# Kernel optimization log

Measured on AMD Instinct MI355X. Metric: run time of the kernel, lower is better.

## Reference

```python
import jax, jax.numpy as jnp
import numpy as np

K = 24            # neighbors
RBF_KERNELS = 16
RBF_GAMMA = 10.0
CUTOFF = 5.0
BN_EPS = 1e-5


def setup_inputs() -> dict:
    key = jax.random.key(0)
    ks = jax.random.split(key, 6)
    B, C, N = 16, 32, 2048
    x = jax.random.normal(ks[0], (B, C, N), dtype=jnp.float32)
    idx_base = (jnp.arange(B, dtype=jnp.int64) * N).reshape(B, 1, 1)
    att_w1 = jax.random.normal(ks[1], (64, 2 * C + RBF_KERNELS), dtype=jnp.float32) * 0.1
    att_w2 = jax.random.normal(ks[2], (1, 64), dtype=jnp.float32) * 0.1
    upd_w = jax.random.normal(ks[3], (64, C), dtype=jnp.float32) * 0.1
    bn_gamma = jnp.ones((64,), dtype=jnp.float32)
    bn_beta = jnp.zeros((64,), dtype=jnp.float32)
    res_w = jax.random.normal(ks[4], (64, C), dtype=jnp.float32) * 0.1
    return {"x": x, "idx_base": idx_base, "att_w1": att_w1, "att_w2": att_w2,
            "upd_w": upd_w, "bn_gamma": bn_gamma, "bn_beta": bn_beta, "res_w": res_w}


def _forward(x, att_w1, att_w2, upd_w, bn_gamma, bn_beta, res_w):
    B, C, N = x.shape
    centers = jnp.linspace(0.0, CUTOFF, RBF_KERNELS).astype(x.dtype)
    # pair[b,i,j] = -||x_i - x_j||^2  (negative squared distance)
    xx = jnp.sum(x * x, axis=1)                          # [B,N]
    dots = jnp.einsum('bcn,bcm->bnm', x, x)              # [B,N,N]
    pair = 2.0 * dots - xx[:, :, None] - xx[:, None, :]
    neg_d2, idx = jax.lax.top_k(pair, K)                 # [B,N,K] nearest neighbors
    dist = jnp.sqrt(jnp.maximum(-neg_d2, 1e-12))         # [B,N,K]
    xt = jnp.transpose(x, (0, 2, 1))                     # [B,N,C]
    neigh = xt[jnp.arange(B)[:, None, None], idx]        # [B,N,K,C] gather
    cent = jnp.broadcast_to(xt[:, :, None, :], (B, N, K, C))
    # RBF expansion of neighbor distances
    diff = dist[..., None] - centers                     # [B,N,K,RBF]
    rbf = jnp.clip(jnp.exp(-RBF_GAMMA * diff * diff), 1e-10, 1.0)
    # attention MLP (1x1 convs == per-edge dense layers)
    att_in = jnp.concatenate([cent, neigh, rbf], axis=-1)          # [B,N,K,2C+RBF]
    h = jax.nn.leaky_relu(jnp.einsum('bnkf,of->bnko', att_in, att_w1), 0.2)
    logits = jnp.einsum('bnko,o->bnk', h, att_w2[0])               # [B,N,K]
    att = jax.nn.softmax(logits, axis=-1)                          # softmax over K neighbors
    weighted = att[..., None] * neigh                              # [B,N,K,C]
    # update_ff: conv1x1 -> BatchNorm2d (batch stats over B,N,K) -> LeakyReLU(0.02)
    upd = jnp.einsum('bnkc,oc->bnko', weighted, upd_w)             # [B,N,K,64]
    mean = jnp.mean(upd, axis=(0, 1, 2))
    var = jnp.mean((upd - mean) ** 2, axis=(0, 1, 2))
    upd = (upd - mean) * jax.lax.rsqrt(var + BN_EPS) * bn_gamma + bn_beta
    upd = jax.nn.leaky_relu(upd, 0.02)
    res = jnp.einsum('bnkc,oc->bnko', neigh, res_w)                # residual projection
    feat = jnp.mean(upd + 0.1 * res, axis=2)                       # mean over K -> [B,N,64]
    return jnp.transpose(feat, (0, 2, 1))                          # [B,64,N]


def reference(x, idx_base, att_w1, att_w2, upd_w, bn_gamma, bn_beta, res_w):
    # idx_base is only needed for torch's flattened-gather trick; the per-batch
    # advanced-index gather above computes identical math.
    return _forward(x, att_w1, att_w2, upd_w, bn_gamma, bn_beta, res_w)
```

## Files before the change

kernel.cpp:

```cpp
#include <hip/hip_runtime.h>
#include <math.h>

#define B_   16
#define C_   32
#define N_   2048
#define K_   24
#define BNK_ (B_*N_*K_)

typedef float vf2 __attribute__((ext_vector_type(2)));
typedef __attribute__((ext_vector_type(8))) short bf16x8;
typedef __attribute__((ext_vector_type(4))) float f32x4;

#define WS_XT   0u
#define WS_XXD  1048576u
#define WS_XXF  1114112u
#define WS_IDX  1146880u
#define WS_D2   1933312u
#define WS_ATT  2719744u
#define WS_LOG  3506176u
#define WS_ST   4292608u
#define WS_AB   4292736u
#define WS_W    4292864u
#define WS_W2   4325632u
#define WS_Y    4358400u
#define WS_L    4358400u
#define WS_HL   10649856u

__device__ __forceinline__ unsigned short bf16rne(float f) {
  unsigned int u = __float_as_uint(f);
  return (unsigned short)((u + 0x7FFFu + ((u >> 16) & 1u)) >> 16);
}

__global__ __launch_bounds__(256) void k0_prep(const float* __restrict__ x,
                                               float* __restrict__ ws) {
  const int i = blockIdx.x;
  const int xcd = i & 7, j = i >> 3;
  const int b = 2 * xcd + (j & 1);
  const int half = j >> 1;
  const int t = (b << 11) + (half << 8) + threadIdx.x;
  const int n = t & 2047;
  const float* xp = x + ((size_t)b * C_ * N_) + n;
  float4* xt4 = (float4*)(ws + WS_XT + (size_t)t * C_);
  uint4*  hl  = (uint4*)(ws + WS_HL) + (size_t)t * 8;
  unsigned int hu[16], lu[16];
  double s = 0.0;
#pragma unroll
  for (int cg = 0; cg < 8; ++cg) {
    float4 v;
    v.x = xp[(size_t)(4*cg  ) * N_];
    v.y = xp[(size_t)(4*cg+1) * N_];
    v.z = xp[(size_t)(4*cg+2) * N_];
    v.w = xp[(size_t)(4*cg+3) * N_];
    xt4[cg] = v;
    s = fma((double)v.x, (double)v.x, s);
    s = fma((double)v.y, (double)v.y, s);
    s = fma((double)v.z, (double)v.z, s);
    s = fma((double)v.w, (double)v.w, s);
    unsigned short h0 = bf16rne(v.x), h1 = bf16rne(v.y);
    unsigned short h2 = bf16rne(v.z), h3 = bf16rne(v.w);
    float l0 = v.x - __uint_as_float((unsigned int)h0 << 16);
    float l1 = v.y - __uint_as_float((unsigned int)h1 << 16);
    float l2 = v.z - __uint_as_float((unsigned int)h2 << 16);
    float l3 = v.w - __uint_as_float((unsigned int)h3 << 16);
    hu[2*cg]   = (unsigned int)h0 | ((unsigned int)h1 << 16);
    hu[2*cg+1] = (unsigned int)h2 | ((unsigned int)h3 << 16);
    lu[2*cg]   = (unsigned int)bf16rne(l0) | ((unsigned int)bf16rne(l1) << 16);
    lu[2*cg+1] = (unsigned int)bf16rne(l2) | ((unsigned int)bf16rne(l3) << 16);
  }
#pragma unroll
  for (int q = 0; q < 4; ++q) {
    uint4 hv; hv.x = hu[4*q]; hv.y = hu[4*q+1]; hv.z = hu[4*q+2]; hv.w = hu[4*q+3];
    hl[q] = hv;
    uint4 lv; lv.x = lu[4*q]; lv.y = lu[4*q+1]; lv.z = lu[4*q+2]; lv.w = lu[4*q+3];
    hl[4+q] = lv;
  }
  ((double*)(ws + WS_XXD))[t] = s;
  ws[WS_XXF + t] = -0.5f * (float)s;
  ws[WS_W + t] = 0.f;
  ws[WS_W2 + t] = 0.f;
  if (t < 128) ws[WS_ST + t] = 0.f;
}

__global__ __launch_bounds__(256, 8) void k1a_mfma(float* __restrict__ ws) {
  __shared__ unsigned short tl[2][1024];
  const int lane = threadIdx.x & 63;
  const int wv   = __builtin_amdgcn_readfirstlane(threadIdx.x >> 6);
  const int i = blockIdx.x;
  const int xcd = i & 7, j = i >> 3;
  const int b = 2 * xcd + (j & 1);
  const int j2 = j >> 1;
  const int nblk = j2 >> 2;
  const int mq   = j2 & 3;
  const int l16 = lane & 15, lg = lane >> 4;

  const unsigned short* HL = (const unsigned short*)(ws + WS_HL) + ((size_t)b << 17);
  const int nrow = (nblk << 6) + (wv << 4) + l16;
  const bf16x8 bh = *(const bf16x8*)(HL + ((size_t)nrow << 6) + (lg << 3));
  const bf16x8 bl = *(const bf16x8*)(HL + ((size_t)nrow << 6) + 32 + (lg << 3));

  const int mbase = mq << 9;
  const float4* nxx = (const float4*)(ws + WS_XXF + (b << 11) + mbase);

  const int srow = lane >> 3;
  const int sslot = (lane & 7) ^ srow;
  const unsigned short* Sp = HL + ((size_t)(mbase + srow) << 6) + (sslot << 3);

  const int ah_off = (l16 << 6) + (((lg    ) ^ (l16 & 7)) << 3);
  const int al_off = (l16 << 6) + (((4 | lg) ^ (l16 & 7)) << 3);

  if (wv == 0) {
    __builtin_amdgcn_global_load_lds(
        (const __attribute__((address_space(1))) unsigned int*)(const void*)Sp,
        (__attribute__((address_space(3))) unsigned int*)(void*)&tl[0][0], 16, 0, 0);
    __builtin_amdgcn_global_load_lds(
        (const __attribute__((address_space(1))) unsigned int*)(const void*)(Sp + 512),
        (__attribute__((address_space(3))) unsigned int*)(void*)&tl[0][512], 16, 0, 0);
  }
  __syncthreads();

  float val[12];
#pragma unroll
  for (int j0 = 0; j0 < 12; ++j0) val[j0] = -3.4e38f;
  int id = mbase + (lg << 2);

#pragma unroll 2
  for (int t = 0; t < 32; ++t) {
    const int cur = t & 1;
    if (t < 31 && wv == (t & 3)) {
      const unsigned short* sp = Sp + ((size_t)(t + 1) << 10);
      __builtin_amdgcn_global_load_lds(
          (const __attribute__((address_space(1))) unsigned int*)(const void*)sp,
          (__attribute__((address_space(3))) unsigned int*)(void*)&tl[cur ^ 1][0], 16, 0, 0);
      __builtin_amdgcn_global_load_lds(
          (const __attribute__((address_space(1))) unsigned int*)(const void*)(sp + 512),
          (__attribute__((address_space(3))) unsigned int*)(void*)&tl[cur ^ 1][512], 16, 0, 0);
    }
    bf16x8 ah = *(const bf16x8*)(&tl[cur][ah_off]);
    bf16x8 al = *(const bf16x8*)(&tl[cur][al_off]);
    float4 xq = nxx[(t << 2) + lg];
    f32x4 acc;
    acc[0] = xq.x; acc[1] = xq.y; acc[2] = xq.z; acc[3] = xq.w;
    acc = __builtin_amdgcn_mfma_f32_16x16x32_bf16(ah, bh, acc, 0, 0, 0);
    acc = __builtin_amdgcn_mfma_f32_16x16x32_bf16(al, bh, acc, 0, 0, 0);
    acc = __builtin_amdgcn_mfma_f32_16x16x32_bf16(ah, bl, acc, 0, 0, 0);
#pragma unroll
    for (int r = 0; r < 4; ++r) {
      int sb = (__float_as_int(acc[r]) & ~2047) | (id + r);
      float sp2 = __int_as_float(sb);
#pragma unroll
      for (int j0 = 11; j0 >= 1; --j0)
        val[j0] = __builtin_amdgcn_fmed3f(val[j0 - 1], val[j0], sp2);
      val[0] = fmaxf(val[0], sp2);
    }
    id += 16;
    __syncthreads();
  }
  const int pg = (b << 5) + nblk;
  float* Lp = ws + WS_L +
      (((size_t)pg * 16 + (mq << 2) + lg) * 12) * 64 + (wv << 4) + l16;
#pragma unroll
  for (int j0 = 0; j0 < 12; ++j0) Lp[(size_t)j0 * 64] = val[j0];
}

__global__ __launch_bounds__(64) void k1b_sel(float* __restrict__ ws) {
  const float* xt = ws + WS_XT;
  const double* xxd = (const double*)(ws + WS_XXD);
  const int lane = threadIdx.x & 63;
  const int i = blockIdx.x;
  const int xcd = i & 7, j = i >> 3;
  const int b = 2 * xcd + (j & 1);
  const int sub = j >> 1;
  const int pg = (b << 5) + sub;
  const int bn = (b << 11) + (sub << 6) + lane;

  float val[28];
#pragma unroll
  for (int j0 = 0; j0 < 28; ++j0) val[j0] = -3.4e38f;
  const float* Lp = ws + WS_L + ((size_t)pg * 16 * 12) * 64 + lane;
#pragma unroll 4
  for (int t = 0; t < 192; ++t) {
    float sp = Lp[(size_t)t * 64];
#pragma unroll
    for (int j0 = 27; j0 >= 1; --j0)
      val[j0] = __builtin_amdgcn_fmed3f(val[j0 - 1], val[j0], sp);
    val[0] = fmaxf(val[0], sp);
  }

  double xnd[C_];
  {
    const float* p = xt + (size_t)bn * C_;
#pragma unroll
    for (int c = 0; c < C_; ++c) xnd[c] = (double)p[c];
  }
  double dl[K_];
#pragma unroll
  for (int j0 = 0; j0 < K_; ++j0) dl[j0] = -1.7e308;

#pragma unroll 1
  for (int j0 = 0; j0 < 28; ++j0) {
    const int m = __float_as_int(val[j0]) & 2047;
    const float* r = xt + ((size_t)((b << 11) + m)) * C_;
    double a0 = 0.0, a1 = 0.0;
#pragma unroll
    for (int c = 0; c < 16; ++c) {
      a0 = fma((double)r[c],      xnd[c],      a0);
      a1 = fma((double)r[c + 16], xnd[c + 16], a1);
    }
    double s = 2.0 * (a0 + a1) - xxd[(b << 11) + m];
    long long bits = (__double_as_longlong(s) & 0xFFFFFFFFFFFFF800ll) | (long long)m;
    double sp = __longlong_as_double(bits);
    if (sp > dl[K_ - 1]) {
      bool c2 = true;
#pragma unroll
      for (int jj = K_ - 1; jj >= 1; --jj) {
        bool c1 = sp > dl[jj - 1];
        dl[jj] = c1 ? dl[jj - 1] : (c2 ? sp : dl[jj]);
        c2 = c1;
      }
      if (c2) dl[0] = sp;
    }
  }

  int*   op = (int*)ws + WS_IDX + (size_t)bn * K_;
  float* dp = ws + WS_D2 + (size_t)bn * K_;
  const double xxn = xxd[bn];
#pragma unroll
  for (int rr = 0; rr < K_; ++rr) {
    long long bl = __double_as_longlong(dl[rr]);
    op[rr] = (int)(bl & 0x7FFll);
    dp[rr] = (float)(xxn - __longlong_as_double(bl & 0xFFFFFFFFFFFFF800ll));
  }
}

__global__ __launch_bounds__(256) void kY(const float* __restrict__ w1,
                                          const float* __restrict__ updw,
                                          const float* __restrict__ resw,
                                          float* __restrict__ ws) {
  const int lane = threadIdx.x & 63;
  const int wv   = __builtin_amdgcn_readfirstlane(threadIdx.x >> 6);
  const int i = blockIdx.x;
  const int xcd = i & 7, j = i >> 3;
  const int b = 2 * xcd + (j & 1);
  const int j2 = j >> 1;
  const int slot = (j2 << 2) | wv;
  const int s  = slot & 7;
  const int pg = slot >> 3;
  const int p = (b << 11) + (pg << 6) + lane;
  const float* xt = ws + WS_XT;

  float row[C_];
  {
    const float4* rp = (const float4*)(xt + (size_t)p * C_);
#pragma unroll
    for (int q = 0; q < 8; ++q) {
      float4 v = rp[q];
      row[4*q] = v.x; row[4*q+1] = v.y; row[4*q+2] = v.z; row[4*q+3] = v.w;
    }
  }
  const int part = s >> 1;
  const int hch  = (s & 1) * 32;
  const float* W   = (part == 0) ? w1 : (part == 1) ? (w1 + 32)
                   : (part == 2) ? updw : resw;
  const int stride = (part < 2) ? 80 : 32;
  float* yp = ws + WS_Y + (size_t)p * 256 + s * 32;
#pragma unroll 2
  for (int og = 0; og < 8; ++og) {
    float a[4] = {0.f, 0.f, 0.f, 0.f};
#pragma unroll
    for (int u = 0; u < 4; ++u) {
      const float* wr = W + (hch + 4 * og + u) * stride;
#pragma unroll
      for (int c = 0; c < C_; ++c) a[u] = fmaf(row[c], wr[c], a[u]);
    }
    float4 st; st.x = a[0]; st.y = a[1]; st.z = a[2]; st.w = a[3];
    ((float4*)yp)[og] = st;
  }
}

__global__ __launch_bounds__(256, 4) void k2_logits(const float* __restrict__ w1,
                                                    const float* __restrict__ w2,
                                                    float* __restrict__ ws) {
  const int lane = threadIdx.x & 63;
  const int wv   = __builtin_amdgcn_readfirstlane(threadIdx.x >> 6);
  const int s = lane & 15, g = lane >> 4;
  const int i = blockIdx.x;
  const int xcd = i & 7, j = i >> 3;
  const int b = 2 * xcd + (j & 1);
  const int grp = j >> 1;
  const int bn = (b << 11) + (grp << 4) + (wv << 2) + g;
  const float* Y = ws + WS_Y;

  float w1r[4][16], w2r[4], ba[4];
#pragma unroll
  for (int e = 0; e < 4; ++e) {
    const int o = 4 * s + e;
    w2r[e] = w2[o];
#pragma unroll
    for (int q = 0; q < 4; ++q) {
      float4 v = *(const float4*)(w1 + o * 80 + 64 + 4 * q);
      w1r[e][4*q] = v.x; w1r[e][4*q+1] = v.y; w1r[e][4*q+2] = v.z; w1r[e][4*q+3] = v.w;
    }
  }
  {
    float4 v = *(const float4*)(Y + (size_t)bn * 256 + 4 * s);
    ba[0] = v.x; ba[1] = v.y; ba[2] = v.z; ba[3] = v.w;
  }

  const int*   ip = (const int*)ws + WS_IDX + (size_t)bn * K_;
  const float* dp = ws + WS_D2 + (size_t)bn * K_;

#pragma unroll 2
  for (int k = 0; k < K_; ++k) {
    const int mk  = ip[k];
    const float dd = dp[k];
    const float dist = sqrtf(fmaxf(dd, 1e-12f));
    float4 rv = *(const float4*)(Y + (size_t)((b << 11) + mk) * 256 + 64 + 4 * s);
    float a0 = ba[0] + rv.x, a1 = ba[1] + rv.y, a2 = ba[2] + rv.z, a3 = ba[3] + rv.w;
#pragma unroll
    for (int r = 0; r < 16; ++r) {
      float t = dist - (float)r * (5.0f / 15.0f);
      float e = __expf(-10.f * t * t);
      float rb = fminf(fmaxf(e, 1e-10f), 1.0f);
      a0 = fmaf(rb, w1r[0][r], a0);
      a1 = fmaf(rb, w1r[1][r], a1);
      a2 = fmaf(rb, w1r[2][r], a2);
      a3 = fmaf(rb, w1r[3][r], a3);
    }
    a0 = fmaxf(a0, 0.2f * a0); a1 = fmaxf(a1, 0.2f * a1);
    a2 = fmaxf(a2, 0.2f * a2); a3 = fmaxf(a3, 0.2f * a3);
    float p = a0 * w2r[0];
    p = fmaf(a1, w2r[1], p);
    p = fmaf(a2, w2r[2], p);
    p = fmaf(a3, w2r[3], p);
    p += __shfl_xor(p, 1);
    p += __shfl_xor(p, 2);
    p += __shfl_xor(p, 4);
    p += __shfl_xor(p, 8);
    if (s == 0) ws[WS_LOG + (size_t)k * 32768 + bn] = p;
  }
}

__global__ __launch_bounds__(256) void k2_softmax(float* __restrict__ ws) {
  __shared__ float h[4096];
  const int i = blockIdx.x;
  const int xcd = i & 7, j = i >> 3;
  const int b = 2 * xcd + (j & 1);
  const int half = j >> 1;
  const int bn = (b << 11) + (half << 8) + threadIdx.x;

#pragma unroll
  for (int q = 0; q < 16; ++q) h[threadIdx.x + (q << 8)] = 0.f;
  __syncthreads();

  float l[K_];
#pragma unroll
  for (int k = 0; k < K_; ++k) l[k] = ws[WS_LOG + (size_t)k * 32768 + bn];
  float mx = l[0];
#pragma unroll
  for (int k = 1; k < K_; ++k) mx = fmaxf(mx, l[k]);
  float den = 0.f;
#pragma unroll
  for (int k = 0; k < K_; ++k) { l[k] = __expf(l[k] - mx); den += l[k]; }
  const float inv = 1.f / den;
#pragma unroll
  for (int k = 0; k < K_; ++k) l[k] *= inv;

  float4* ap = (float4*)(ws + WS_ATT + (size_t)bn * K_);
#pragma unroll
  for (int q = 0; q < 6; ++q) {
    float4 v; v.x = l[4*q]; v.y = l[4*q+1]; v.z = l[4*q+2]; v.w = l[4*q+3];
    ap[q] = v;
  }
  const int* ip = (const int*)ws + WS_IDX + (size_t)bn * K_;
#pragma unroll
  for (int k = 0; k < K_; ++k) {
    const int mk = ip[k];
    atomicAdd(&h[mk], l[k]);
    atomicAdd(&h[2048 + mk], l[k] * l[k]);
  }
  __syncthreads();
#pragma unroll
  for (int q = 0; q < 8; ++q) {
    const int m = threadIdx.x + (q << 8);
    atomicAdd(ws + WS_W  + (b << 11) + m, h[m]);
    atomicAdd(ws + WS_W2 + (b << 11) + m, h[2048 + m]);
  }
}

__global__ __launch_bounds__(256) void k2b_stats(float* __restrict__ ws) {
  __shared__ float ls[128];
  const int lane = threadIdx.x & 63;
  const int wv   = __builtin_amdgcn_readfirstlane(threadIdx.x >> 6);
  if (threadIdx.x < 128) ls[threadIdx.x] = 0.f;
  __syncthreads();
  const int i = blockIdx.x;
  const int xcd = i & 7, j = i >> 3;
  const int b = 2 * xcd + (j & 1);
  const int half = j >> 1;
  const float* Y = ws + WS_Y;
  float s1 = 0.f, s2 = 0.f;
#pragma unroll 1
  for (int it = 0; it < 64; ++it) {
    const int m = (b << 11) + (half << 8) + (wv << 6) + it;
    const float w  = ws[WS_W + m];
    const float w2 = ws[WS_W2 + m];
    const float yv = Y[(size_t)m * 256 + 128 + lane];
    s1 = fmaf(w, yv, s1);
    s2 = fmaf(w2, yv * yv, s2);
  }
  atomicAdd(&ls[lane], s1);
  atomicAdd(&ls[64 + lane], s2);
  __syncthreads();
  if (threadIdx.x < 128) atomicAdd(ws + WS_ST + threadIdx.x, ls[threadIdx.x]);
}

__global__ __launch_bounds__(256) void k4_out(float* __restrict__ out,
                                              const float* __restrict__ gam,
                                              const float* __restrict__ bet,
                                              const float* __restrict__ ws) {
  __shared__ float tile[32][65];
  const int lane = threadIdx.x & 63;
  const int wv   = __builtin_amdgcn_readfirstlane(threadIdx.x >> 6);
  const int i = blockIdx.x;
  const int xcd = i & 7, j = i >> 3;
  const int b = 2 * xcd + (j & 1);
  const int j2 = j >> 1;
  const int n0 = j2 << 5;
  const float* Y = ws + WS_Y;

  float A, Bb;
  {
    const float s1 = ws[WS_ST + lane], s2 = ws[WS_ST + 64 + lane];
    const float cnt = (float)BNK_;
    const float mean = s1 / cnt;
    const float var = fmaxf(s2 / cnt - mean * mean, 0.f);
    A = gam[lane] / sqrtf(var + 1e-5f);
    Bb = bet[lane] - mean * A;
  }

#pragma unroll 1
  for (int pt = 0; pt < 8; ++pt) {
    const int bn = (b << 11) + n0 + (wv << 3) + pt;
    const int*   ip = (const int*)ws + WS_IDX + (size_t)bn * K_;
    const float* ap = ws + WS_ATT + (size_t)bn * K_;
    float facc = 0.f, racc = 0.f;
#pragma unroll
    for (int k = 0; k < K_; ++k) {
      const int mk = ip[k];
      const float* row = Y + (size_t)((b << 11) + mk) * 256;
      float yv = row[128 + lane];
      float rv = row[192 + lane];
      float u = ap[k] * yv;
      float v = fmaf(u, A, Bb);
      v = v > 0.f ? v : 0.02f * v;
      facc += v;
      racc += rv;
    }
    tile[(wv << 3) + pt][lane] = (facc + 0.1f * racc) * (1.f / 24.f);
  }
  __syncthreads();
  const int o = threadIdx.x >> 2, q = threadIdx.x & 3;
  float* op = out + ((size_t)(b * 64 + o)) * 2048 + n0 + q * 8;
  float4 v0, v1;
  v0.x = tile[q*8+0][o]; v0.y = tile[q*8+1][o]; v0.z = tile[q*8+2][o]; v0.w = tile[q*8+3][o];
  v1.x = tile[q*8+4][o]; v1.y = tile[q*8+5][o]; v1.z = tile[q*8+6][o]; v1.w = tile[q*8+7][o];
  ((float4*)op)[0] = v0;
  ((float4*)op)[1] = v1;
}

extern "C" void kernel_launch(void* const* d_in, const int* in_sizes, int n_in,
                              void* d_out, int out_size, void* d_ws, size_t ws_size,
                              hipStream_t stream) {
  (void)in_sizes; (void)n_in; (void)out_size; (void)ws_size;
  const float* x    = (const float*)d_in[0];
  const float* w1   = (const float*)d_in[2];
  const float* w2   = (const float*)d_in[3];
  const float* updw = (const float*)d_in[4];
  const float* bng  = (const float*)d_in[5];
  const float* bnb  = (const float*)d_in[6];
  const float* resw = (const float*)d_in[7];
  float* out = (float*)d_out;
  float* ws  = (float*)d_ws;

  k0_prep  <<<dim3(128),  dim3(256), 0, stream>>>(x, ws);
  k1a_mfma <<<dim3(2048), dim3(256), 0, stream>>>(ws);
  k1b_sel  <<<dim3(512),  dim3(64),  0, stream>>>(ws);
  kY       <<<dim3(1024), dim3(256), 0, stream>>>(w1, updw, resw, ws);
  k2_logits<<<dim3(2048), dim3(256), 0, stream>>>(w1, w2, ws);
  k2_softmax<<<dim3(128), dim3(256), 0, stream>>>(ws);
  k2b_stats<<<dim3(128),  dim3(256), 0, stream>>>(ws);
  k4_out   <<<dim3(1024), dim3(256), 0, stream>>>(out, bng, bnb, ws);
}
```

Baseline: 348.2 us.

## Deduplicate RBF expansion in logits kernel via per-wave shared memory

k2_logits is remapped so each lane owns one of the 64 hidden channels and a wave handles its 4 points one after another. Each point's 24×16 RBF values are computed once per wave, stored in LDS and read back as float4 broadcasts. Before, the 16 lanes serving a point each recomputed every exp, so this removes that redundant transcendental work and cuts register use. It costs a longer serial loop per wave, a full 64-lane shuffle reduction per neighbor, and reliance on in-wave LDS ordering with no barrier; occupancy is also raised to 8 blocks per CU.

```diff
diff --git a/kernel.cpp b/kernel.cpp
--- a/kernel.cpp
+++ b/kernel.cpp
@@ -277,66 +277,68 @@
   }
 }
 
-__global__ __launch_bounds__(256, 4) void k2_logits(const float* __restrict__ w1,
+__global__ __launch_bounds__(256, 8) void k2_logits(const float* __restrict__ w1,
                                                     const float* __restrict__ w2,
                                                     float* __restrict__ ws) {
+  __shared__ float dist_s[4][24];
+  __shared__ float rbf_s[4][384];
   const int lane = threadIdx.x & 63;
   const int wv   = __builtin_amdgcn_readfirstlane(threadIdx.x >> 6);
-  const int s = lane & 15, g = lane >> 4;
   const int i = blockIdx.x;
   const int xcd = i & 7, j = i >> 3;
   const int b = 2 * xcd + (j & 1);
   const int grp = j >> 1;
-  const int bn = (b << 11) + (grp << 4) + (wv << 2) + g;
   const float* Y = ws + WS_Y;
 
-  float w1r[4][16], w2r[4], ba[4];
-#pragma unroll
-  for (int e = 0; e < 4; ++e) {
-    const int o = 4 * s + e;
-    w2r[e] = w2[o];
+  float w1r[16], w2r;
+  {
+    const float4* wp = (const float4*)(w1 + lane * 80 + 64);
 #pragma unroll
     for (int q = 0; q < 4; ++q) {
-      float4 v = *(const float4*)(w1 + o * 80 + 64 + 4 * q);
-      w1r[e][4*q] = v.x; w1r[e][4*q+1] = v.y; w1r[e][4*q+2] = v.z; w1r[e][4*q+3] = v.w;
-    }
-  }
-  {
-    float4 v = *(const float4*)(Y + (size_t)bn * 256 + 4 * s);
-    ba[0] = v.x; ba[1] = v.y; ba[2] = v.z; ba[3] = v.w;
-  }
-
-  const int*   ip = (const int*)ws + WS_IDX + (size_t)bn * K_;
-  const float* dp = ws + WS_D2 + (size_t)bn * K_;
-
+      float4 v = wp[q];
+      w1r[4*q] = v.x; w1r[4*q+1] = v.y; w1r[4*q+2] = v.z; w1r[4*q+3] = v.w;
+    }
+    w2r = w2[lane];
+  }
+
+#pragma unroll 1
+  for (int q = 0; q < 4; ++q) {
+    const int bn = (b << 11) + (grp << 4) + (wv << 2) + q;
+    const int*   ip  = (const int*)ws + WS_IDX + (size_t)bn * K_;
+    const float* dpp = ws + WS_D2 + (size_t)bn * K_;
+    if (lane < K_) dist_s[wv][lane] = sqrtf(fmaxf(dpp[lane], 1e-12f));
+#pragma unroll
+    for (int t = 0; t < 6; ++t) {
+      const int f = lane + (t << 6);
+      const int k = f >> 4, r = f & 15;
+      float d = dist_s[wv][k];
+      float tt = d - (float)r * (5.0f / 15.0f);
+      float e = __expf(-10.f * tt * tt);
+      rbf_s[wv][f] = fminf(fmaxf(e, 1e-10f), 1.0f);
+    }
+    const float ba = Y[(size_t)bn * 256 + lane];
 #pragma unroll 2
-  for (int k = 0; k < K_; ++k) {
-    const int mk  = ip[k];
-    const float dd = dp[k];
-    const float dist = sqrtf(fmaxf(dd, 1e-12f));
-    float4 rv = *(const float4*)(Y + (size_t)((b << 11) + mk) * 256 + 64 + 4 * s);
-    float a0 = ba[0] + rv.x, a1 = ba[1] + rv.y, a2 = ba[2] + rv.z, a3 = ba[3] + rv.w;
-#pragma unroll
-    for (int r = 0; r < 16; ++r) {
-      float t = dist - (float)r * (5.0f / 15.0f);
-      float e = __expf(-10.f * t * t);
-      float rb = fminf(fmaxf(e, 1e-10f), 1.0f);
-      a0 = fmaf(rb, w1r[0][r], a0);
-      a1 = fmaf(rb, w1r[1][r], a1);
-      a2 = fmaf(rb, w1r[2][r], a2);
-      a3 = fmaf(rb, w1r[3][r], a3);
-    }
-    a0 = fmaxf(a0, 0.2f * a0); a1 = fmaxf(a1, 0.2f * a1);
-    a2 = fmaxf(a2, 0.2f * a2); a3 = fmaxf(a3, 0.2f * a3);
-    float p = a0 * w2r[0];
-    p = fmaf(a1, w2r[1], p);
-    p = fmaf(a2, w2r[2], p);
-    p = fmaf(a3, w2r[3], p);
-    p += __shfl_xor(p, 1);
-    p += __shfl_xor(p, 2);
-    p += __shfl_xor(p, 4);
-    p += __shfl_xor(p, 8);
-    if (s == 0) ws[WS_LOG + (size_t)k * 32768 + bn] = p;
+    for (int k = 0; k < K_; ++k) {
+      const int mk = ip[k];
+      float rv = Y[(size_t)((b << 11) + mk) * 256 + 64 + lane];
+      const float4* rp = (const float4*)&rbf_s[wv][k << 4];
+      float4 r0 = rp[0], r1 = rp[1], r2 = rp[2], r3 = rp[3];
+      float acc = ba + rv;
+      acc = fmaf(r0.x, w1r[0],  acc); acc = fmaf(r0.y, w1r[1],  acc);
+      acc = fmaf(r0.z, w1r[2],  acc); acc = fmaf(r0.w, w1r[3],  acc);
+      acc = fmaf(r1.x, w1r[4],  acc); acc = fmaf(r1.y, w1r[5],  acc);
+      acc = fmaf(r1.z, w1r[6],  acc); acc = fmaf(r1.w, w1r[7],  acc);
+      acc = fmaf(r2.x, w1r[8],  acc); acc = fmaf(r2.y, w1r[9],  acc);
+      acc = fmaf(r2.z, w1r[10], acc); acc = fmaf(r2.w, w1r[11], acc);
+      acc = fmaf(r3.x, w1r[12], acc); acc = fmaf(r3.y, w1r[13], acc);
+      acc = fmaf(r3.z, w1r[14], acc); acc = fmaf(r3.w, w1r[15], acc);
+      acc = fmaxf(acc, 0.2f * acc);
+      float p = acc * w2r;
+      p += __shfl_xor(p, 1);  p += __shfl_xor(p, 2);
+      p += __shfl_xor(p, 4);  p += __shfl_xor(p, 8);
+      p += __shfl_xor(p, 16); p += __shfl_xor(p, 32);
+      if (lane == 0) ws[WS_LOG + (size_t)k * 32768 + bn] = p;
+    }
   }
 }
 
```

Measured after the change: 352.8 us. Within noise of the previous version (+1.3%).
